# Performance work log

Measured on AMD Instinct MI355X. Metric: run time of the kernel, lower is better.

Reference implementation:

```python
import jax, jax.numpy as jnp
import numpy as np

L = 4  # num GIN layers
HID = 128
B_GRAPHS = 4096

def _bn(x, g, b, m, v):
    return (x - m) / jnp.sqrt(v + 1e-5) * g + b

def _ln(x, g, b):
    mu = jnp.mean(x, axis=-1, keepdims=True)
    var = jnp.var(x, axis=-1, keepdims=True)
    return (x - mu) / jnp.sqrt(var + 1e-5) * g + b

def _gin_encoder(x, ei, bat, aW, ab, eps, W1, b1, g1, be1, m1, v1, W2, b2, g2, be2, m2, v2):
    # x: [N,9], ei: [2,E], bat: [N]
    h = x @ aW + ab                                   # [N,HID]
    src, dst = ei[0], ei[1]
    for l in range(L):
        agg = jnp.zeros_like(h).at[dst].add(h[src])   # scatter-add neighbor sum
        z = (1.0 + eps[l]) * h + agg
        z = jax.nn.relu(_bn(z @ W1[l] + b1[l], g1[l], be1[l], m1[l], v1[l]))
        z = z @ W2[l] + b2[l]
        h = jax.nn.relu(_bn(z, g2[l], be2[l], m2[l], v2[l]))
    sums = jax.ops.segment_sum(h, bat, num_segments=B_GRAPHS)
    cnt = jax.ops.segment_sum(jnp.ones((h.shape[0],), h.dtype), bat, num_segments=B_GRAPHS)
    return sums / jnp.maximum(cnt, 1.0)[:, None]      # global_mean_pool -> [B,HID]

def reference(dx, de, db, sx, se, sb, t,
              enc_atom_W, enc_atom_b, enc_eps, enc_W1, enc_b1,
              enc_bn1_g, enc_bn1_b, enc_bn1_m, enc_bn1_v,
              enc_W2, enc_b2, enc_bn_g, enc_bn_b, enc_bn_m, enc_bn_v,
              temp_W1, temp_b1, temp_W2, temp_b2,
              int_W, int_b, int_ln_g, int_ln_b,
              fus_W1, fus_b1, fus_ln1_g, fus_ln1_b,
              fus_W2, fus_b2, fus_ln2_g, fus_ln2_b, fus_W3, fus_b3):
    # three encoders: [aq(drug), bs(drug), solvent], stacked on leading axis
    xs = jnp.stack([dx, dx, sx])      # [3,N,9]
    eis = jnp.stack([de, de, se])     # [3,2,E]
    bats = jnp.stack([db, db, sb])    # [3,N]
    embs = jax.vmap(_gin_encoder)(xs, eis, bats,
                                  enc_atom_W, enc_atom_b, enc_eps, enc_W1, enc_b1,
                                  enc_bn1_g, enc_bn1_b, enc_bn1_m, enc_bn1_v,
                                  enc_W2, enc_b2, enc_bn_g, enc_bn_b, enc_bn_m, enc_bn_v)
    aq, bs_, so = embs[0], embs[1], embs[2]           # each [B,HID]
    inter = jax.nn.relu(_ln(jnp.concatenate([bs_, so], axis=1) @ int_W + int_b, int_ln_g, int_ln_b))
    temp = jax.nn.relu(t @ temp_W1 + temp_b1) @ temp_W2 + temp_b2
    fusion = jnp.concatenate([aq, inter, temp], axis=1)  # [B, 2*HID+32]
    h = jax.nn.relu(_ln(fusion @ fus_W1 + fus_b1, fus_ln1_g, fus_ln1_b))
    h = jax.nn.relu(_ln(h @ fus_W2 + fus_b2, fus_ln2_g, fus_ln2_b))
    return h @ fus_W3 + fus_b3                        # [B,1]

def setup_inputs() -> dict:
    key = jax.random.key(0)
    ks = jax.random.split(key, 16)
    N, E, B = 50000, 600000, B_GRAPHS
    s = 0.1  # weight scale
    inp = {
        'dx': jax.random.normal(ks[0], (N, 9), jnp.float32),
        'de': jax.random.randint(ks[1], (2, E), 0, N),
        'db': jnp.sort(jax.random.randint(ks[2], (N,), 0, B)),
        'sx': jax.random.normal(ks[3], (N, 9), jnp.float32),
        'se': jax.random.randint(ks[4], (2, E), 0, N),
        'sb': jnp.sort(jax.random.randint(ks[5], (N,), 0, B)),
        't': jax.random.normal(ks[6], (B, 1), jnp.float32),
        'enc_atom_W': jax.random.normal(ks[7], (3, 9, HID), jnp.float32) * s,
        'enc_atom_b': jnp.zeros((3, HID), jnp.float32),
        'enc_eps': jnp.zeros((3, L), jnp.float32),
        'enc_W1': jax.random.normal(ks[8], (3, L, HID, 2 * HID), jnp.float32) * s,
        'enc_b1': jnp.zeros((3, L, 2 * HID), jnp.float32),
        'enc_bn1_g': jnp.ones((3, L, 2 * HID), jnp.float32),
        'enc_bn1_b': jnp.zeros((3, L, 2 * HID), jnp.float32),
        'enc_bn1_m': jnp.zeros((3, L, 2 * HID), jnp.float32),
        'enc_bn1_v': jnp.ones((3, L, 2 * HID), jnp.float32),
        'enc_W2': jax.random.normal(ks[9], (3, L, 2 * HID, HID), jnp.float32) * s,
        'enc_b2': jnp.zeros((3, L, HID), jnp.float32),
        'enc_bn_g': jnp.ones((3, L, HID), jnp.float32),
        'enc_bn_b': jnp.zeros((3, L, HID), jnp.float32),
        'enc_bn_m': jnp.zeros((3, L, HID), jnp.float32),
        'enc_bn_v': jnp.ones((3, L, HID), jnp.float32),
        'temp_W1': jax.random.normal(ks[10], (1, 32), jnp.float32) * s,
        'temp_b1': jnp.zeros((32,), jnp.float32),
        'temp_W2': jax.random.normal(ks[11], (32, 32), jnp.float32) * s,
        'temp_b2': jnp.zeros((32,), jnp.float32),
        'int_W': jax.random.normal(ks[12], (2 * HID, HID), jnp.float32) * s,
        'int_b': jnp.zeros((HID,), jnp.float32),
        'int_ln_g': jnp.ones((HID,), jnp.float32),
        'int_ln_b': jnp.zeros((HID,), jnp.float32),
        'fus_W1': jax.random.normal(ks[13], (2 * HID + 32, HID), jnp.float32) * s,
        'fus_b1': jnp.zeros((HID,), jnp.float32),
        'fus_ln1_g': jnp.ones((HID,), jnp.float32),
        'fus_ln1_b': jnp.zeros((HID,), jnp.float32),
        'fus_W2': jax.random.normal(ks[14], (HID, HID // 2), jnp.float32) * s,
        'fus_b2': jnp.zeros((HID // 2,), jnp.float32),
        'fus_ln2_g': jnp.ones((HID // 2,), jnp.float32),
        'fus_ln2_b': jnp.zeros((HID // 2,), jnp.float32),
        'fus_W3': jax.random.normal(ks[15], (HID // 2, 1), jnp.float32) * s,
        'fus_b3': jnp.zeros((1,), jnp.float32),
    }
    return inp
```

## Files before the change

### kernel.cpp

```cpp
#include <hip/hip_runtime.h>

#define HID 128
#define NLAYER 4

typedef unsigned short u16;
typedef __attribute__((ext_vector_type(8))) unsigned short u16x8;
typedef __attribute__((ext_vector_type(8))) short short8;
typedef __attribute__((ext_vector_type(4))) float floatx4;

__device__ __forceinline__ float bf2f(u16 u) {
    union { unsigned int i; float f; } v; v.i = ((unsigned int)u) << 16; return v.f;
}
__device__ __forceinline__ u16 f2bf(float f) {
    union { float f; unsigned int i; } v; v.f = f;
    unsigned int r = v.i + 0x7FFFu + ((v.i >> 16) & 1u);
    return (u16)(r >> 16);
}

__device__ __forceinline__ int lowbound(const int* __restrict__ a, int n, int v) {
    int lo = 0, hi = n;
    while (lo < hi) {
        int mid = (lo + hi) >> 1;
        if (a[mid] < v) lo = mid + 1; else hi = mid;
    }
    return lo;
}

__global__ void prep_weights(const float* __restrict__ W1, const float* __restrict__ W2,
                             u16* __restrict__ W1t, u16* __restrict__ W2t) {
    const int T = 3 * NLAYER * 128 * 256;
    int o = blockIdx.x * blockDim.x + threadIdx.x;
    if (o < T) {
        int k = o & 127, n = (o >> 7) & 255, el = o >> 15;
        W1t[o] = f2bf(W1[((size_t)el * 128 + k) * 256 + n]);
    } else if (o < 2 * T) {
        int o2 = o - T;
        int k = o2 & 255, n = (o2 >> 8) & 127, el = o2 >> 15;
        W2t[o2] = f2bf(W2[((size_t)el * 256 + k) * 128 + n]);
    }
}

__global__ void hist2(const int* __restrict__ de, const int* __restrict__ se,
                      int* __restrict__ cntd, int* __restrict__ cnts, int Ed, int Es) {
    const int g = blockIdx.y;
    const int* ei = g ? se : de;
    int* cnt = g ? cnts : cntd;
    const int E = g ? Es : Ed;
    int e = blockIdx.x * 256 + threadIdx.x;
    if (e < E) atomicAdd(&cnt[ei[E + e]], 1);
}

__global__ __launch_bounds__(256) void scan1v(const int* __restrict__ cntd,
                                              const int* __restrict__ cnts,
                                              int* __restrict__ bsumd,
                                              int* __restrict__ bsums, int N) {
    const int g = blockIdx.y;
    const int* cnt = g ? cnts : cntd;
    int* bsum = g ? bsums : bsumd;
    __shared__ int s[256];
    int i = blockIdx.x * 256 + threadIdx.x;
    s[threadIdx.x] = (i < N) ? cnt[i] : 0;
    __syncthreads();
    for (int o = 128; o > 0; o >>= 1) {
        if (threadIdx.x < o) s[threadIdx.x] += s[threadIdx.x + o];
        __syncthreads();
    }
    if (threadIdx.x == 0) bsum[blockIdx.x] = s[0];
}

__global__ __launch_bounds__(256) void scan2v(int* __restrict__ bsumd,
                                              int* __restrict__ bsums, int nb) {
    int* bsum = blockIdx.x ? bsums : bsumd;
    __shared__ int s[256];
    __shared__ int carry;
    if (threadIdx.x == 0) carry = 0;
    __syncthreads();
    for (int base = 0; base < nb; base += 256) {
        int i = base + threadIdx.x;
        int v = (i < nb) ? bsum[i] : 0;
        s[threadIdx.x] = v;
        __syncthreads();
        for (int o = 1; o < 256; o <<= 1) {
            int tv = (threadIdx.x >= o) ? s[threadIdx.x - o] : 0;
            __syncthreads();
            s[threadIdx.x] += tv;
            __syncthreads();
        }
        int excl = carry + s[threadIdx.x] - v;
        if (i < nb) bsum[i] = excl;
        __syncthreads();
        if (threadIdx.x == 0) carry += s[255];
        __syncthreads();
    }
}

__global__ __launch_bounds__(256) void scan3v(const int* __restrict__ cntd,
                                              const int* __restrict__ cnts,
                                              const int* __restrict__ bsumd,
                                              const int* __restrict__ bsums,
                                              int* __restrict__ rpd, int* __restrict__ rps,
                                              int* __restrict__ curd, int* __restrict__ curs,
                                              int N, int Ed, int Es) {
    const int g = blockIdx.y;
    const int* cnt = g ? cnts : cntd;
    const int* bsum = g ? bsums : bsumd;
    int* rowptr = g ? rps : rpd;
    int* cur = g ? curs : curd;
    const int E = g ? Es : Ed;
    __shared__ int s[256];
    int i = blockIdx.x * 256 + threadIdx.x;
    int v = (i < N) ? cnt[i] : 0;
    s[threadIdx.x] = v;
    __syncthreads();
    for (int o = 1; o < 256; o <<= 1) {
        int tv = (threadIdx.x >= o) ? s[threadIdx.x - o] : 0;
        __syncthreads();
        s[threadIdx.x] += tv;
        __syncthreads();
    }
    if (i < N) {
        const int st = bsum[blockIdx.x] + s[threadIdx.x] - v;
        rowptr[i] = st;
        cur[i] = st;
    }
    if (i == 0 && blockIdx.x == 0) rowptr[N] = E;
}

__global__ __launch_bounds__(256) void fill2b(const int* __restrict__ de,
                                              const int* __restrict__ se,
                                              int* __restrict__ curd, int* __restrict__ curs,
                                              int* __restrict__ sid, int* __restrict__ sis,
                                              int Ed, int Es, int N) {
    const int g = blockIdx.y;
    const int* ei = g ? se : de;
    int* cur = g ? curs : curd;
    int* srcidx = g ? sis : sid;
    const int E = g ? Es : Ed;
    const int nchunk = gridDim.x >> 3;
    const int bin = blockIdx.x & 7;
    const int chunk = blockIdx.x >> 3;
    const int BS = (N + 7) >> 3;
    const int dlo = bin * BS;
    const int dhi = min(N, dlo + BS);
    const int ce = (E + nchunk - 1) / nchunk;
    const int elo = chunk * ce;
    const int ehi = min(E, elo + ce);
    for (int e = elo + (int)threadIdx.x; e < ehi; e += 256) {
        const int dst = ei[E + e];
        if (dst >= dlo && dst < dhi) {
            const int pos = atomicAdd(&cur[dst], 1);
            srcidx[pos] = ei[e];
        }
    }
}

__global__ void atom_kernel(const float* __restrict__ dx, const float* __restrict__ sx,
                            const float* __restrict__ aW, const float* __restrict__ ab,
                            u16* __restrict__ h, int N) {
    const int slot = blockIdx.z;
    long idx = (long)blockIdx.x * blockDim.x + threadIdx.x;
    if (idx >= (long)N * HID) return;
    const int n = (int)(idx / HID), c = (int)(idx % HID);
    const float* x = (slot < 2) ? dx : sx;
    const float* W = aW + (size_t)slot * 9 * HID;
    float acc = ab[slot * HID + c];
#pragma unroll
    for (int k = 0; k < 9; k++) acc = fmaf(x[n * 9 + k], W[k * HID + c], acc);
    h[(size_t)slot * N * HID + idx] = f2bf(acc);
}

__global__ __launch_bounds__(256) void gather_agg(
    const int* __restrict__ rpd, const int* __restrict__ sid,
    const int* __restrict__ rps, const int* __restrict__ sis,
    const u16* __restrict__ h, u16* __restrict__ z,
    const float* __restrict__ eps, int N, int l) {
    const int slot = blockIdx.z;
    const int node = blockIdx.x * 16 + (threadIdx.x >> 4);
    if (node >= N) return;
    const int lane = threadIdx.x & 63;
    const int sl = lane & 15;
    const int subbase = lane & 48;
    const int* rowptr = (slot < 2) ? rpd : rps;
    const int* srcidx = (slot < 2) ? sid : sis;
    const int lo = rowptr[node], hi = rowptr[node + 1];
    const u16* hp = h + (size_t)slot * N * HID;
    const int coff = sl * 8;

    u16x8 hv = *(const u16x8*)(hp + (size_t)node * HID + coff);
    const float scale = 1.f + eps[slot * NLAYER + l];
    float s[8];
#pragma unroll
    for (int i = 0; i < 8; i++) s[i] = bf2f(hv[i]) * scale;

    for (int base = lo; base < hi; base += 16) {
        const int cnt = min(16, hi - base);
        int idx = (sl < cnt) ? srcidx[base + sl] : 0;
        int j = 0;
        for (; j + 4 <= cnt; j += 4) {
            const int s0 = __shfl(idx, subbase + j);
            const int s1 = __shfl(idx, subbase + j + 1);
            const int s2 = __shfl(idx, subbase + j + 2);
            const int s3 = __shfl(idx, subbase + j + 3);
            u16x8 v0 = *(const u16x8*)(hp + (size_t)s0 * HID + coff);
            u16x8 v1 = *(const u16x8*)(hp + (size_t)s1 * HID + coff);
            u16x8 v2 = *(const u16x8*)(hp + (size_t)s2 * HID + coff);
            u16x8 v3 = *(const u16x8*)(hp + (size_t)s3 * HID + coff);
#pragma unroll
            for (int i = 0; i < 8; i++)
                s[i] += (bf2f(v0[i]) + bf2f(v1[i])) + (bf2f(v2[i]) + bf2f(v3[i]));
        }
        for (; j < cnt; j++) {
            const int sj = __shfl(idx, subbase + j);
            u16x8 v = *(const u16x8*)(hp + (size_t)sj * HID + coff);
#pragma unroll
            for (int i = 0; i < 8; i++) s[i] += bf2f(v[i]);
        }
    }
    u16x8 o;
#pragma unroll
    for (int i = 0; i < 8; i++) o[i] = f2bf(s[i]);
    *(u16x8*)(z + (size_t)slot * N * HID + (size_t)node * HID + coff) = o;
}

__global__ __launch_bounds__(256, 2) void fused_layer(
    const u16* __restrict__ A, const u16* __restrict__ W1t, const u16* __restrict__ W2t,
    const float* __restrict__ b1, const float* __restrict__ g1, const float* __restrict__ be1,
    const float* __restrict__ m1, const float* __restrict__ v1,
    const float* __restrict__ b2, const float* __restrict__ g2, const float* __restrict__ be2,
    const float* __restrict__ m2, const float* __restrict__ v2,
    u16* __restrict__ out, int M, int l) {

    const int slot = blockIdx.z;
    const int m0 = blockIdx.x * 128;
    const u16* Ap  = A + (size_t)slot * M * 128;
    const int el = slot * NLAYER + l;
    const u16* Wp1 = W1t + (size_t)el * (256 * 128);
    const u16* Wp2 = W2t + (size_t)el * (128 * 256);
    const size_t poff1 = (size_t)el * 256;
    const size_t poff2 = (size_t)el * 128;

    __shared__ u16 sm[128 * 136];

    const int tid = threadIdx.x;
    const int lane = tid & 63;
    const int w = tid >> 6;
    const int sl = lane & 15;
    const int k8 = lane >> 4;

    {
        const int rp = tid >> 4;
        const int kc = (tid & 15) * 8;
#pragma unroll
        for (int p = 0; p < 8; p++) {
            const int row = p * 16 + rp;
            int gr = m0 + row; if (gr >= M) gr = M - 1;
            *(uint4*)&sm[row * 136 + kc] = *(const uint4*)(Ap + (size_t)gr * 128 + kc);
        }
    }
    __syncthreads();

    floatx4 acc1[8][4];
#pragma unroll
    for (int mt = 0; mt < 8; mt++)
#pragma unroll
        for (int c = 0; c < 4; c++) acc1[mt][c] = (floatx4)0.f;

#pragma unroll
    for (int ks = 0; ks < 4; ks++) {
        short8 a[8], b[4];
#pragma unroll
        for (int mt = 0; mt < 8; mt++)
            a[mt] = *(const short8*)&sm[(mt * 16 + sl) * 136 + ks * 32 + k8 * 8];
#pragma unroll
        for (int c = 0; c < 4; c++) {
            const int n = (c * 4 + w) * 16 + sl;
            b[c] = *(const short8*)(Wp1 + (size_t)n * 128 + ks * 32 + k8 * 8);
        }
#pragma unroll
        for (int mt = 0; mt < 8; mt++)
#pragma unroll
            for (int c = 0; c < 4; c++)
                acc1[mt][c] = __builtin_amdgcn_mfma_f32_16x16x32_bf16(a[mt], b[c], acc1[mt][c], 0, 0, 0);
    }
    __syncthreads();

    const int wr = w & 1, wc = w >> 1;
    floatx4 acc2[4][4];
#pragma unroll
    for (int mt = 0; mt < 4; mt++)
#pragma unroll
        for (int nt = 0; nt < 4; nt++) acc2[mt][nt] = (floatx4)0.f;

#pragma unroll
    for (int part = 0; part < 2; part++) {
#pragma unroll
        for (int c = part * 2; c < part * 2 + 2; c++) {
            const int gcol = (c * 4 + w) * 16 + sl;
            const int lcol = gcol - part * 128;
            const float sc = g1[poff1 + gcol] * rsqrtf(v1[poff1 + gcol] + 1e-5f);
            const float sh = (b1[poff1 + gcol] - m1[poff1 + gcol]) * sc + be1[poff1 + gcol];
#pragma unroll
            for (int mt = 0; mt < 8; mt++) {
#pragma unroll
                for (int r = 0; r < 4; r++) {
                    const int m = mt * 16 + k8 * 4 + r;
                    sm[m * 136 + lcol] = f2bf(fmaxf(fmaf(acc1[mt][c][r], sc, sh), 0.f));
                }
            }
        }
        __syncthreads();
#pragma unroll
        for (int ks = 0; ks < 4; ks++) {
            short8 a[4], b[4];
#pragma unroll
            for (int mt = 0; mt < 4; mt++)
                a[mt] = *(const short8*)&sm[(wr * 64 + mt * 16 + sl) * 136 + ks * 32 + k8 * 8];
#pragma unroll
            for (int nt = 0; nt < 4; nt++) {
                const int n = wc * 64 + nt * 16 + sl;
                b[nt] = *(const short8*)(Wp2 + (size_t)n * 256 + part * 128 + ks * 32 + k8 * 8);
            }
#pragma unroll
            for (int mt = 0; mt < 4; mt++)
#pragma unroll
                for (int nt = 0; nt < 4; nt++)
                    acc2[mt][nt] = __builtin_amdgcn_mfma_f32_16x16x32_bf16(a[mt], b[nt], acc2[mt][nt], 0, 0, 0);
        }
        if (part == 0) __syncthreads();
    }

    u16* outp = out + (size_t)slot * M * 128;
#pragma unroll
    for (int nt = 0; nt < 4; nt++) {
        const int col = wc * 64 + nt * 16 + sl;
        const float sc = g2[poff2 + col] * rsqrtf(v2[poff2 + col] + 1e-5f);
        const float sh = (b2[poff2 + col] - m2[poff2 + col]) * sc + be2[poff2 + col];
#pragma unroll
        for (int mt = 0; mt < 4; mt++) {
#pragma unroll
            for (int r = 0; r < 4; r++) {
                const int gr = m0 + wr * 64 + mt * 16 + k8 * 4 + r;
                if (gr < M)
                    outp[(size_t)gr * 128 + col] = f2bf(fmaxf(fmaf(acc2[mt][nt][r], sc, sh), 0.f));
            }
        }
    }
}

__global__ __launch_bounds__(128) void pool_kernel(const int* __restrict__ db,
                                                   const int* __restrict__ sb,
                                                   const u16* __restrict__ h,
                                                   float* __restrict__ emb,
                                                   int N, int B) {
    const int slot = blockIdx.z;
    const int* bat = (slot < 2) ? db : sb;
    const int g = blockIdx.x;
    const int lo = lowbound(bat, N, g);
    const int hi = lowbound(bat, N, g + 1);
    const int c = threadIdx.x;
    float s = 0.f;
    const u16* hp = h + (size_t)slot * N * HID;
    for (int n = lo; n < hi; n++) s += bf2f(hp[(size_t)n * HID + c]);
    const float cnt = (float)(hi - lo);
    emb[((size_t)slot * B + g) * HID + c] = s / fmaxf(cnt, 1.f);
}

__device__ __forceinline__ float block_sum128(float x, float* red, int tid) {
    red[tid] = x;
    __syncthreads();
    if (tid < 64) {
        float v = red[tid] + red[tid + 64];
#pragma unroll
        for (int o = 32; o > 0; o >>= 1) v += __shfl_down(v, o);
        if (tid == 0) red[0] = v;
    }
    __syncthreads();
    float r = red[0];
    __syncthreads();
    return r;
}

__global__ __launch_bounds__(128) void fusion_kernel(
    const float* __restrict__ emb, const float* __restrict__ t,
    const float* __restrict__ tW1, const float* __restrict__ tb1,
    const float* __restrict__ tW2, const float* __restrict__ tb2,
    const float* __restrict__ iW, const float* __restrict__ ib,
    const float* __restrict__ ilg, const float* __restrict__ ilb,
    const float* __restrict__ fW1, const float* __restrict__ fb1,
    const float* __restrict__ l1g, const float* __restrict__ l1b,
    const float* __restrict__ fW2, const float* __restrict__ fb2,
    const float* __restrict__ l2g, const float* __restrict__ l2b,
    const float* __restrict__ fW3, const float* __restrict__ fb3,
    float* __restrict__ out, int B) {
    const int r = blockIdx.x;
    const int tid = threadIdx.x;
    __shared__ float cs[256];
    __shared__ float cat[288];
    __shared__ float buf[128];
    __shared__ float red[128];
    __shared__ float tmp32[32];

    cs[tid]        = emb[((size_t)1 * B + r) * HID + tid];
    cs[128 + tid]  = emb[((size_t)2 * B + r) * HID + tid];
    cat[tid]       = emb[((size_t)0 * B + r) * HID + tid];
    __syncthreads();

    float acc = ib[tid];
    for (int k = 0; k < 256; k++) acc = fmaf(cs[k], iW[k * HID + tid], acc);
    float mu  = block_sum128(acc, red, tid) * (1.f / 128.f);
    float d   = acc - mu;
    float var = block_sum128(d * d, red, tid) * (1.f / 128.f);
    float inter = fmaxf(d * rsqrtf(var + 1e-5f) * ilg[tid] + ilb[tid], 0.f);
    cat[128 + tid] = inter;

    if (tid < 32) tmp32[tid] = fmaxf(fmaf(t[r], tW1[tid], tb1[tid]), 0.f);
    __syncthreads();
    if (tid < 32) {
        float a2 = tb2[tid];
        for (int j = 0; j < 32; j++) a2 = fmaf(tmp32[j], tW2[j * 32 + tid], a2);
        cat[256 + tid] = a2;
    }
    __syncthreads();

    float a1 = fb1[tid];
    for (int k = 0; k < 288; k++) a1 = fmaf(cat[k], fW1[k * HID + tid], a1);
    mu  = block_sum128(a1, red, tid) * (1.f / 128.f);
    d   = a1 - mu;
    var = block_sum128(d * d, red, tid) * (1.f / 128.f);
    buf[tid] = fmaxf(d * rsqrtf(var + 1e-5f) * l1g[tid] + l1b[tid], 0.f);
    __syncthreads();

    float a2v = 0.f;
    if (tid < 64) {
        a2v = fb2[tid];
        for (int k = 0; k < 128; k++) a2v = fmaf(buf[k], fW2[k * 64 + tid], a2v);
    }
    mu = block_sum128((tid < 64) ? a2v : 0.f, red, tid) * (1.f / 64.f);
    float d2 = (tid < 64) ? (a2v - mu) : 0.f;
    var = block_sum128(d2 * d2, red, tid) * (1.f / 64.f);
    float contrib = 0.f;
    if (tid < 64) {
        float h2 = fmaxf(d2 * rsqrtf(var + 1e-5f) * l2g[tid] + l2b[tid], 0.f);
        contrib = h2 * fW3[tid];
    }
    float s = block_sum128(contrib, red, tid);
    if (tid == 0) out[r] = s + fb3[0];
}

extern "C" void kernel_launch(void* const* d_in, const int* in_sizes, int n_in,
                              void* d_out, int out_size, void* d_ws, size_t ws_size,
                              hipStream_t stream) {
    const float* dx  = (const float*)d_in[0];
    const int*   de  = (const int*)d_in[1];
    const int*   db  = (const int*)d_in[2];
    const float* sx  = (const float*)d_in[3];
    const int*   se  = (const int*)d_in[4];
    const int*   sb  = (const int*)d_in[5];
    const float* t   = (const float*)d_in[6];
    const float* aW  = (const float*)d_in[7];
    const float* ab  = (const float*)d_in[8];
    const float* eps = (const float*)d_in[9];
    const float* W1  = (const float*)d_in[10];
    const float* b1  = (const float*)d_in[11];
    const float* g1  = (const float*)d_in[12];
    const float* be1 = (const float*)d_in[13];
    const float* m1  = (const float*)d_in[14];
    const float* v1  = (const float*)d_in[15];
    const float* W2  = (const float*)d_in[16];
    const float* b2  = (const float*)d_in[17];
    const float* g2  = (const float*)d_in[18];
    const float* be2 = (const float*)d_in[19];
    const float* m2  = (const float*)d_in[20];
    const float* v2  = (const float*)d_in[21];
    const float* tW1 = (const float*)d_in[22];
    const float* tb1 = (const float*)d_in[23];
    const float* tW2 = (const float*)d_in[24];
    const float* tb2 = (const float*)d_in[25];
    const float* iW  = (const float*)d_in[26];
    const float* ib  = (const float*)d_in[27];
    const float* ilg = (const float*)d_in[28];
    const float* ilb = (const float*)d_in[29];
    const float* fW1 = (const float*)d_in[30];
    const float* fb1 = (const float*)d_in[31];
    const float* l1g = (const float*)d_in[32];
    const float* l1b = (const float*)d_in[33];
    const float* fW2 = (const float*)d_in[34];
    const float* fb2 = (const float*)d_in[35];
    const float* l2g = (const float*)d_in[36];
    const float* l2b = (const float*)d_in[37];
    const float* fW3 = (const float*)d_in[38];
    const float* fb3 = (const float*)d_in[39];
    float* out = (float*)d_out;

    const int N  = in_sizes[0] / 9;
    const int Ed = in_sizes[1] / 2;
    const int Es = in_sizes[4] / 2;
    const int B  = in_sizes[6];
    const int nb = (N + 255) / 256;

    char* w8 = (char*)d_ws;
    int* rpd   = (int*)w8;
    int* rps   = rpd + (N + 1);
    int* cntd  = rps + (N + 1);
    int* cnts  = cntd + N;
    int* curd  = cnts + N;
    int* curs  = curd + N;
    int* sid   = curs + N;
    int* sis   = sid + Ed;
    int* bsumd = sis + Es;
    int* bsums = bsumd + nb;
    size_t int_bytes = ((char*)(bsums + nb)) - w8;
    size_t foff = (int_bytes + 255) & ~(size_t)255;

    const int WT = 3 * NLAYER * 128 * 256;
    u16* W1t = (u16*)(w8 + foff);
    u16* W2t = W1t + WT;
    const size_t hS = (size_t)N * HID;
    u16* hbuf = W2t + WT;
    u16* zbuf = hbuf + 3 * hS;
    float* emb = (float*)(((uintptr_t)(zbuf + 3 * hS) + 255) & ~(uintptr_t)255);

    prep_weights<<<(2 * WT + 255) / 256, 256, 0, stream>>>(W1, W2, W1t, W2t);
    hipMemsetAsync(cntd, 0, (size_t)2 * N * sizeof(int), stream);
    {
        const int Emax = (Ed > Es) ? Ed : Es;
        dim3 gh((Emax + 255) / 256, 2);
        hist2<<<gh, 256, 0, stream>>>(de, se, cntd, cnts, Ed, Es);
        dim3 gs1(nb, 2);
        scan1v<<<gs1, 256, 0, stream>>>(cntd, cnts, bsumd, bsums, N);
        scan2v<<<2, 256, 0, stream>>>(bsumd, bsums, nb);
        scan3v<<<gs1, 256, 0, stream>>>(cntd, cnts, bsumd, bsums, rpd, rps, curd, curs, N, Ed, Es);
        dim3 gfb(128 * 8, 2);
        fill2b<<<gfb, 256, 0, stream>>>(de, se, curd, curs, sid, sis, Ed, Es, N);
    }

    {
        dim3 ga((N * HID + 255) / 256, 1, 3);
        atom_kernel<<<ga, 256, 0, stream>>>(dx, sx, aW, ab, hbuf, N);
        for (int l = 0; l < NLAYER; l++) {
            dim3 gg((N + 15) / 16, 1, 3);
            gather_agg<<<gg, 256, 0, stream>>>(rpd, sid, rps, sis, hbuf, zbuf, eps, N, l);
            dim3 gf((N + 127) / 128, 1, 3);
            fused_layer<<<gf, 256, 0, stream>>>(zbuf, W1t, W2t,
                                                b1, g1, be1, m1, v1,
                                                b2, g2, be2, m2, v2,
                                                hbuf, N, l);
        }
        dim3 gp(B, 1, 3);
        pool_kernel<<<gp, 128, 0, stream>>>(db, sb, hbuf, emb, N, B);
    }
    fusion_kernel<<<B, 128, 0, stream>>>(emb, t, tW1, tb1, tW2, tb2,
                                         iW, ib, ilg, ilb, fW1, fb1, l1g, l1b,
                                         fW2, fb2, l2g, l2b, fW3, fb3, out, B);
}
```

Baseline: 826.5 us.

## Interleave the two drug encoders' features so one gather serves both slots

Node features for the two drug encoders, which share the same graph, are stored interleaved as 256-wide rows. The aggregation kernel now walks the drug CSR once and sums both encoders' neighbour rows in a single pass, while solvent nodes are handled in a second z-slice. This removes the duplicate index reads and traversal for the shared drug graph and makes each neighbour fetch a contiguous 512-byte row. The dense layer and pooling kernels take a row stride to read and write this layout. The cost is more registers per thread and a 2-way unroll instead of 4-way in the drug path.

```diff
diff --git a/kernel.cpp b/kernel.cpp
--- a/kernel.cpp
+++ b/kernel.cpp
@@ -156,7 +156,7 @@
 
 __global__ void atom_kernel(const float* __restrict__ dx, const float* __restrict__ sx,
                             const float* __restrict__ aW, const float* __restrict__ ab,
-                            u16* __restrict__ h, int N) {
+                            u16* __restrict__ h01, u16* __restrict__ h2, int N) {
     const int slot = blockIdx.z;
     long idx = (long)blockIdx.x * blockDim.x + threadIdx.x;
     if (idx >= (long)N * HID) return;
@@ -166,73 +166,121 @@
     float acc = ab[slot * HID + c];
 #pragma unroll
     for (int k = 0; k < 9; k++) acc = fmaf(x[n * 9 + k], W[k * HID + c], acc);
-    h[(size_t)slot * N * HID + idx] = f2bf(acc);
-}
-
-__global__ __launch_bounds__(256) void gather_agg(
+    if (slot < 2) h01[(size_t)n * 256 + slot * 128 + c] = f2bf(acc);
+    else          h2[(size_t)n * 128 + c] = f2bf(acc);
+}
+
+__global__ __launch_bounds__(256) void gather_agg2(
     const int* __restrict__ rpd, const int* __restrict__ sid,
     const int* __restrict__ rps, const int* __restrict__ sis,
-    const u16* __restrict__ h, u16* __restrict__ z,
+    const u16* __restrict__ h01, const u16* __restrict__ h2,
+    u16* __restrict__ z01, u16* __restrict__ z2,
     const float* __restrict__ eps, int N, int l) {
-    const int slot = blockIdx.z;
+    const int pz = blockIdx.z;
     const int node = blockIdx.x * 16 + (threadIdx.x >> 4);
     if (node >= N) return;
     const int lane = threadIdx.x & 63;
     const int sl = lane & 15;
     const int subbase = lane & 48;
-    const int* rowptr = (slot < 2) ? rpd : rps;
-    const int* srcidx = (slot < 2) ? sid : sis;
-    const int lo = rowptr[node], hi = rowptr[node + 1];
-    const u16* hp = h + (size_t)slot * N * HID;
     const int coff = sl * 8;
 
-    u16x8 hv = *(const u16x8*)(hp + (size_t)node * HID + coff);
-    const float scale = 1.f + eps[slot * NLAYER + l];
-    float s[8];
-#pragma unroll
-    for (int i = 0; i < 8; i++) s[i] = bf2f(hv[i]) * scale;
-
-    for (int base = lo; base < hi; base += 16) {
-        const int cnt = min(16, hi - base);
-        int idx = (sl < cnt) ? srcidx[base + sl] : 0;
-        int j = 0;
-        for (; j + 4 <= cnt; j += 4) {
-            const int s0 = __shfl(idx, subbase + j);
-            const int s1 = __shfl(idx, subbase + j + 1);
-            const int s2 = __shfl(idx, subbase + j + 2);
-            const int s3 = __shfl(idx, subbase + j + 3);
-            u16x8 v0 = *(const u16x8*)(hp + (size_t)s0 * HID + coff);
-            u16x8 v1 = *(const u16x8*)(hp + (size_t)s1 * HID + coff);
-            u16x8 v2 = *(const u16x8*)(hp + (size_t)s2 * HID + coff);
-            u16x8 v3 = *(const u16x8*)(hp + (size_t)s3 * HID + coff);
-#pragma unroll
-            for (int i = 0; i < 8; i++)
-                s[i] += (bf2f(v0[i]) + bf2f(v1[i])) + (bf2f(v2[i]) + bf2f(v3[i]));
-        }
-        for (; j < cnt; j++) {
-            const int sj = __shfl(idx, subbase + j);
-            u16x8 v = *(const u16x8*)(hp + (size_t)sj * HID + coff);
-#pragma unroll
-            for (int i = 0; i < 8; i++) s[i] += bf2f(v[i]);
-        }
-    }
-    u16x8 o;
-#pragma unroll
-    for (int i = 0; i < 8; i++) o[i] = f2bf(s[i]);
-    *(u16x8*)(z + (size_t)slot * N * HID + (size_t)node * HID + coff) = o;
+    if (pz == 0) {
+        const int lo = rpd[node], hi = rpd[node + 1];
+        const float sc0 = 1.f + eps[0 * NLAYER + l];
+        const float sc1 = 1.f + eps[1 * NLAYER + l];
+        float s0[8], s1[8];
+        {
+            u16x8 a0 = *(const u16x8*)(h01 + (size_t)node * 256 + coff);
+            u16x8 a1 = *(const u16x8*)(h01 + (size_t)node * 256 + 128 + coff);
+#pragma unroll
+            for (int i = 0; i < 8; i++) { s0[i] = bf2f(a0[i]) * sc0; s1[i] = bf2f(a1[i]) * sc1; }
+        }
+        for (int base = lo; base < hi; base += 16) {
+            const int cnt = min(16, hi - base);
+            int idx = (sl < cnt) ? sid[base + sl] : 0;
+            int j = 0;
+            for (; j + 2 <= cnt; j += 2) {
+                const int e0 = __shfl(idx, subbase + j);
+                const int e1 = __shfl(idx, subbase + j + 1);
+                u16x8 v00 = *(const u16x8*)(h01 + (size_t)e0 * 256 + coff);
+                u16x8 v01 = *(const u16x8*)(h01 + (size_t)e0 * 256 + 128 + coff);
+                u16x8 v10 = *(const u16x8*)(h01 + (size_t)e1 * 256 + coff);
+                u16x8 v11 = *(const u16x8*)(h01 + (size_t)e1 * 256 + 128 + coff);
+#pragma unroll
+                for (int i = 0; i < 8; i++) {
+                    s0[i] += bf2f(v00[i]) + bf2f(v10[i]);
+                    s1[i] += bf2f(v01[i]) + bf2f(v11[i]);
+                }
+            }
+            for (; j < cnt; j++) {
+                const int e0 = __shfl(idx, subbase + j);
+                u16x8 v0 = *(const u16x8*)(h01 + (size_t)e0 * 256 + coff);
+                u16x8 v1 = *(const u16x8*)(h01 + (size_t)e0 * 256 + 128 + coff);
+#pragma unroll
+                for (int i = 0; i < 8; i++) { s0[i] += bf2f(v0[i]); s1[i] += bf2f(v1[i]); }
+            }
+        }
+        u16x8 o0, o1;
+#pragma unroll
+        for (int i = 0; i < 8; i++) { o0[i] = f2bf(s0[i]); o1[i] = f2bf(s1[i]); }
+        *(u16x8*)(z01 + (size_t)node * 256 + coff) = o0;
+        *(u16x8*)(z01 + (size_t)node * 256 + 128 + coff) = o1;
+    } else {
+        const int lo = rps[node], hi = rps[node + 1];
+        const float scale = 1.f + eps[2 * NLAYER + l];
+        float s[8];
+        {
+            u16x8 hv = *(const u16x8*)(h2 + (size_t)node * 128 + coff);
+#pragma unroll
+            for (int i = 0; i < 8; i++) s[i] = bf2f(hv[i]) * scale;
+        }
+        for (int base = lo; base < hi; base += 16) {
+            const int cnt = min(16, hi - base);
+            int idx = (sl < cnt) ? sis[base + sl] : 0;
+            int j = 0;
+            for (; j + 4 <= cnt; j += 4) {
+                const int e0 = __shfl(idx, subbase + j);
+                const int e1 = __shfl(idx, subbase + j + 1);
+                const int e2 = __shfl(idx, subbase + j + 2);
+                const int e3 = __shfl(idx, subbase + j + 3);
+                u16x8 v0 = *(const u16x8*)(h2 + (size_t)e0 * 128 + coff);
+                u16x8 v1 = *(const u16x8*)(h2 + (size_t)e1 * 128 + coff);
+                u16x8 v2 = *(const u16x8*)(h2 + (size_t)e2 * 128 + coff);
+                u16x8 v3 = *(const u16x8*)(h2 + (size_t)e3 * 128 + coff);
+#pragma unroll
+                for (int i = 0; i < 8; i++)
+                    s[i] += (bf2f(v0[i]) + bf2f(v1[i])) + (bf2f(v2[i]) + bf2f(v3[i]));
+            }
+            for (; j < cnt; j++) {
+                const int e0 = __shfl(idx, subbase + j);
+                u16x8 v = *(const u16x8*)(h2 + (size_t)e0 * 128 + coff);
+#pragma unroll
+                for (int i = 0; i < 8; i++) s[i] += bf2f(v[i]);
+            }
+        }
+        u16x8 o;
+#pragma unroll
+        for (int i = 0; i < 8; i++) o[i] = f2bf(s[i]);
+        *(u16x8*)(z2 + (size_t)node * 128 + coff) = o;
+    }
 }
 
 __global__ __launch_bounds__(256, 2) void fused_layer(
-    const u16* __restrict__ A, const u16* __restrict__ W1t, const u16* __restrict__ W2t,
+    const u16* __restrict__ A01, const u16* __restrict__ A2,
+    const u16* __restrict__ W1t, const u16* __restrict__ W2t,
     const float* __restrict__ b1, const float* __restrict__ g1, const float* __restrict__ be1,
     const float* __restrict__ m1, const float* __restrict__ v1,
     const float* __restrict__ b2, const float* __restrict__ g2, const float* __restrict__ be2,
     const float* __restrict__ m2, const float* __restrict__ v2,
-    u16* __restrict__ out, int M, int l) {
+    u16* __restrict__ out01, u16* __restrict__ out2, int M, int l) {
 
     const int slot = blockIdx.z;
     const int m0 = blockIdx.x * 128;
-    const u16* Ap  = A + (size_t)slot * M * 128;
+    const u16* Ap;
+    u16* outp;
+    int rs;
+    if (slot < 2) { Ap = A01 + slot * 128; outp = out01 + slot * 128; rs = 256; }
+    else          { Ap = A2;               outp = out2;               rs = 128; }
     const int el = slot * NLAYER + l;
     const u16* Wp1 = W1t + (size_t)el * (256 * 128);
     const u16* Wp2 = W2t + (size_t)el * (128 * 256);
@@ -254,7 +302,7 @@
         for (int p = 0; p < 8; p++) {
             const int row = p * 16 + rp;
             int gr = m0 + row; if (gr >= M) gr = M - 1;
-            *(uint4*)&sm[row * 136 + kc] = *(const uint4*)(Ap + (size_t)gr * 128 + kc);
+            *(uint4*)&sm[row * 136 + kc] = *(const uint4*)(Ap + (size_t)gr * rs + kc);
         }
     }
     __syncthreads();
@@ -329,7 +377,6 @@
         if (part == 0) __syncthreads();
     }
 
-    u16* outp = out + (size_t)slot * M * 128;
 #pragma unroll
     for (int nt = 0; nt < 4; nt++) {
         const int col = wc * 64 + nt * 16 + sl;
@@ -341,7 +388,7 @@
             for (int r = 0; r < 4; r++) {
                 const int gr = m0 + wr * 64 + mt * 16 + k8 * 4 + r;
                 if (gr < M)
-                    outp[(size_t)gr * 128 + col] = f2bf(fmaxf(fmaf(acc2[mt][nt][r], sc, sh), 0.f));
+                    outp[(size_t)gr * rs + col] = f2bf(fmaxf(fmaf(acc2[mt][nt][r], sc, sh), 0.f));
             }
         }
     }
@@ -349,7 +396,8 @@
 
 __global__ __launch_bounds__(128) void pool_kernel(const int* __restrict__ db,
                                                    const int* __restrict__ sb,
-                                                   const u16* __restrict__ h,
+                                                   const u16* __restrict__ h01,
+                                                   const u16* __restrict__ h2,
                                                    float* __restrict__ emb,
                                                    int N, int B) {
     const int slot = blockIdx.z;
@@ -359,8 +407,12 @@
     const int hi = lowbound(bat, N, g + 1);
     const int c = threadIdx.x;
     float s = 0.f;
-    const u16* hp = h + (size_t)slot * N * HID;
-    for (int n = lo; n < hi; n++) s += bf2f(hp[(size_t)n * HID + c]);
+    if (slot < 2) {
+        const u16* hp = h01 + slot * 128;
+        for (int n = lo; n < hi; n++) s += bf2f(hp[(size_t)n * 256 + c]);
+    } else {
+        for (int n = lo; n < hi; n++) s += bf2f(h2[(size_t)n * 128 + c]);
+    }
     const float cnt = (float)(hi - lo);
     emb[((size_t)slot * B + g) * HID + c] = s / fmaxf(cnt, 1.f);
 }
@@ -536,18 +588,22 @@
 
     {
         dim3 ga((N * HID + 255) / 256, 1, 3);
-        atom_kernel<<<ga, 256, 0, stream>>>(dx, sx, aW, ab, hbuf, N);
+        atom_kernel<<<ga, 256, 0, stream>>>(dx, sx, aW, ab, hbuf, hbuf + 2 * hS, N);
+        u16* cur = hbuf;
+        u16* nxt = zbuf;
         for (int l = 0; l < NLAYER; l++) {
-            dim3 gg((N + 15) / 16, 1, 3);
-            gather_agg<<<gg, 256, 0, stream>>>(rpd, sid, rps, sis, hbuf, zbuf, eps, N, l);
+            dim3 gg((N + 15) / 16, 1, 2);
+            gather_agg2<<<gg, 256, 0, stream>>>(rpd, sid, rps, sis,
+                                                cur, cur + 2 * hS,
+                                                nxt, nxt + 2 * hS, eps, N, l);
             dim3 gf((N + 127) / 128, 1, 3);
-            fused_layer<<<gf, 256, 0, stream>>>(zbuf, W1t, W2t,
+            fused_layer<<<gf, 256, 0, stream>>>(nxt, nxt + 2 * hS, W1t, W2t,
                                                 b1, g1, be1, m1, v1,
                                                 b2, g2, be2, m2, v2,
-                                                hbuf, N, l);
+                                                cur, cur + 2 * hS, N, l);
         }
         dim3 gp(B, 1, 3);
-        pool_kernel<<<gp, 128, 0, stream>>>(db, sb, hbuf, emb, N, B);
+        pool_kernel<<<gp, 128, 0, stream>>>(db, sb, hbuf, hbuf + 2 * hS, emb, N, B);
     }
     fusion_kernel<<<B, 128, 0, stream>>>(emb, t, tW1, tb1, tW2, tb2,
                                          iW, ib, ilg, ilb, fW1, fb1, l1g, l1b,
```

Measured after the change: 874.4 us. 1.06x slower.

## Halve fused_layer row tile and interleave GEMM1 halves to cut registers

Applied to the files above, without the earlier changes.

The fused MLP layer kernel now processes 64 rows per block instead of 128 and computes the first GEMM in two 128-column halves, each immediately feeding the second GEMM, with separate shared buffers for the input tile and the hidden activations. This shrinks accumulator register usage (acc1 8x4 down to 4x2, acc2 4x4 down to 2x4), so the launch bound rises to 4 blocks per SM and the grid doubles. The aim is higher occupancy and more blocks for latency hiding. The cost is that each weight tile is reloaded from global or cache memory twice as often per row.

```diff
diff --git a/kernel.cpp b/kernel.cpp
--- a/kernel.cpp
+++ b/kernel.cpp
@@ -222,7 +222,7 @@
     *(u16x8*)(z + (size_t)slot * N * HID + (size_t)node * HID + coff) = o;
 }
 
-__global__ __launch_bounds__(256, 2) void fused_layer(
+__global__ __launch_bounds__(256, 4) void fused_layer(
     const u16* __restrict__ A, const u16* __restrict__ W1t, const u16* __restrict__ W2t,
     const float* __restrict__ b1, const float* __restrict__ g1, const float* __restrict__ be1,
     const float* __restrict__ m1, const float* __restrict__ v1,
@@ -231,7 +231,7 @@
     u16* __restrict__ out, int M, int l) {
 
     const int slot = blockIdx.z;
-    const int m0 = blockIdx.x * 128;
+    const int m0 = blockIdx.x * 64;
     const u16* Ap  = A + (size_t)slot * M * 128;
     const int el = slot * NLAYER + l;
     const u16* Wp1 = W1t + (size_t)el * (256 * 128);
@@ -239,7 +239,8 @@
     const size_t poff1 = (size_t)el * 256;
     const size_t poff2 = (size_t)el * 128;
 
-    __shared__ u16 sm[128 * 136];
+    __shared__ u16 smz[64 * 136];
+    __shared__ u16 smz2[64 * 136];
 
     const int tid = threadIdx.x;
     const int lane = tid & 63;
@@ -251,80 +252,80 @@
         const int rp = tid >> 4;
         const int kc = (tid & 15) * 8;
 #pragma unroll
-        for (int p = 0; p < 8; p++) {
+        for (int p = 0; p < 4; p++) {
             const int row = p * 16 + rp;
             int gr = m0 + row; if (gr >= M) gr = M - 1;
-            *(uint4*)&sm[row * 136 + kc] = *(const uint4*)(Ap + (size_t)gr * 128 + kc);
-        }
-    }
-    __syncthreads();
-
-    floatx4 acc1[8][4];
-#pragma unroll
-    for (int mt = 0; mt < 8; mt++)
-#pragma unroll
-        for (int c = 0; c < 4; c++) acc1[mt][c] = (floatx4)0.f;
-
-#pragma unroll
-    for (int ks = 0; ks < 4; ks++) {
-        short8 a[8], b[4];
-#pragma unroll
-        for (int mt = 0; mt < 8; mt++)
-            a[mt] = *(const short8*)&sm[(mt * 16 + sl) * 136 + ks * 32 + k8 * 8];
-#pragma unroll
-        for (int c = 0; c < 4; c++) {
-            const int n = (c * 4 + w) * 16 + sl;
-            b[c] = *(const short8*)(Wp1 + (size_t)n * 128 + ks * 32 + k8 * 8);
-        }
-#pragma unroll
-        for (int mt = 0; mt < 8; mt++)
-#pragma unroll
-            for (int c = 0; c < 4; c++)
-                acc1[mt][c] = __builtin_amdgcn_mfma_f32_16x16x32_bf16(a[mt], b[c], acc1[mt][c], 0, 0, 0);
+            *(uint4*)&smz[row * 136 + kc] = *(const uint4*)(Ap + (size_t)gr * 128 + kc);
+        }
     }
     __syncthreads();
 
     const int wr = w & 1, wc = w >> 1;
-    floatx4 acc2[4][4];
-#pragma unroll
-    for (int mt = 0; mt < 4; mt++)
+    floatx4 acc2[2][4];
+#pragma unroll
+    for (int mt = 0; mt < 2; mt++)
 #pragma unroll
         for (int nt = 0; nt < 4; nt++) acc2[mt][nt] = (floatx4)0.f;
 
 #pragma unroll
     for (int part = 0; part < 2; part++) {
-#pragma unroll
-        for (int c = part * 2; c < part * 2 + 2; c++) {
-            const int gcol = (c * 4 + w) * 16 + sl;
+        floatx4 acc1[4][2];
+#pragma unroll
+        for (int mt = 0; mt < 4; mt++)
+#pragma unroll
+            for (int cc = 0; cc < 2; cc++) acc1[mt][cc] = (floatx4)0.f;
+
+#pragma unroll
+        for (int ks = 0; ks < 4; ks++) {
+            short8 a[4], b[2];
+#pragma unroll
+            for (int mt = 0; mt < 4; mt++)
+                a[mt] = *(const short8*)&smz[(mt * 16 + sl) * 136 + ks * 32 + k8 * 8];
+#pragma unroll
+            for (int cc = 0; cc < 2; cc++) {
+                const int n = ((part * 2 + cc) * 4 + w) * 16 + sl;
+                b[cc] = *(const short8*)(Wp1 + (size_t)n * 128 + ks * 32 + k8 * 8);
+            }
+#pragma unroll
+            for (int mt = 0; mt < 4; mt++)
+#pragma unroll
+                for (int cc = 0; cc < 2; cc++)
+                    acc1[mt][cc] = __builtin_amdgcn_mfma_f32_16x16x32_bf16(a[mt], b[cc], acc1[mt][cc], 0, 0, 0);
+        }
+
+#pragma unroll
+        for (int cc = 0; cc < 2; cc++) {
+            const int gcol = ((part * 2 + cc) * 4 + w) * 16 + sl;
             const int lcol = gcol - part * 128;
             const float sc = g1[poff1 + gcol] * rsqrtf(v1[poff1 + gcol] + 1e-5f);
             const float sh = (b1[poff1 + gcol] - m1[poff1 + gcol]) * sc + be1[poff1 + gcol];
 #pragma unroll
-            for (int mt = 0; mt < 8; mt++) {
+            for (int mt = 0; mt < 4; mt++) {
 #pragma unroll
                 for (int r = 0; r < 4; r++) {
                     const int m = mt * 16 + k8 * 4 + r;
-                    sm[m * 136 + lcol] = f2bf(fmaxf(fmaf(acc1[mt][c][r], sc, sh), 0.f));
+                    smz2[m * 136 + lcol] = f2bf(fmaxf(fmaf(acc1[mt][cc][r], sc, sh), 0.f));
                 }
             }
         }
         __syncthreads();
+
 #pragma unroll
         for (int ks = 0; ks < 4; ks++) {
-            short8 a[4], b[4];
-#pragma unroll
-            for (int mt = 0; mt < 4; mt++)
-                a[mt] = *(const short8*)&sm[(wr * 64 + mt * 16 + sl) * 136 + ks * 32 + k8 * 8];
+            short8 a2[2], b2[4];
+#pragma unroll
+            for (int mt = 0; mt < 2; mt++)
+                a2[mt] = *(const short8*)&smz2[(wr * 32 + mt * 16 + sl) * 136 + ks * 32 + k8 * 8];
 #pragma unroll
             for (int nt = 0; nt < 4; nt++) {
                 const int n = wc * 64 + nt * 16 + sl;
-                b[nt] = *(const short8*)(Wp2 + (size_t)n * 256 + part * 128 + ks * 32 + k8 * 8);
+                b2[nt] = *(const short8*)(Wp2 + (size_t)n * 256 + part * 128 + ks * 32 + k8 * 8);
             }
 #pragma unroll
-            for (int mt = 0; mt < 4; mt++)
+            for (int mt = 0; mt < 2; mt++)
 #pragma unroll
                 for (int nt = 0; nt < 4; nt++)
-                    acc2[mt][nt] = __builtin_amdgcn_mfma_f32_16x16x32_bf16(a[mt], b[nt], acc2[mt][nt], 0, 0, 0);
+                    acc2[mt][nt] = __builtin_amdgcn_mfma_f32_16x16x32_bf16(a2[mt], b2[nt], acc2[mt][nt], 0, 0, 0);
         }
         if (part == 0) __syncthreads();
     }
@@ -336,10 +337,10 @@
         const float sc = g2[poff2 + col] * rsqrtf(v2[poff2 + col] + 1e-5f);
         const float sh = (b2[poff2 + col] - m2[poff2 + col]) * sc + be2[poff2 + col];
 #pragma unroll
-        for (int mt = 0; mt < 4; mt++) {
+        for (int mt = 0; mt < 2; mt++) {
 #pragma unroll
             for (int r = 0; r < 4; r++) {
-                const int gr = m0 + wr * 64 + mt * 16 + k8 * 4 + r;
+                const int gr = m0 + wr * 32 + mt * 16 + k8 * 4 + r;
                 if (gr < M)
                     outp[(size_t)gr * 128 + col] = f2bf(fmaxf(fmaf(acc2[mt][nt][r], sc, sh), 0.f));
             }
@@ -540,7 +541,7 @@
         for (int l = 0; l < NLAYER; l++) {
             dim3 gg((N + 15) / 16, 1, 3);
             gather_agg<<<gg, 256, 0, stream>>>(rpd, sid, rps, sis, hbuf, zbuf, eps, N, l);
-            dim3 gf((N + 127) / 128, 1, 3);
+            dim3 gf((N + 63) / 64, 1, 3);
             fused_layer<<<gf, 256, 0, stream>>>(zbuf, W1t, W2t,
                                                 b1, g1, be1, m1, v1,
                                                 b2, g2, be2, m2, v2,
```

Result: slower. 933.8 us (+13.0%).

## Stage GEMM weights through LDS and bin histogram atomics by destination range

Applied to the files above, without the earlier changes.

The fused layer kernel now loads W1 and W2 tiles cooperatively into a padded shared-memory buffer before the MFMA loops, instead of having each wave read B fragments straight from global memory. This is meant to cut redundant global and L2 weight traffic. The cost is more LDS per block, which may lower occupancy, plus extra barriers. Separately, the degree histogram is rewritten to use 8 destination bins over edge chunks, like fill2b, so atomics stay within a node range. That bin split makes each edge get read 8 times.

```diff
diff --git a/kernel.cpp b/kernel.cpp
--- a/kernel.cpp
+++ b/kernel.cpp
@@ -40,14 +40,27 @@
     }
 }
 
-__global__ void hist2(const int* __restrict__ de, const int* __restrict__ se,
-                      int* __restrict__ cntd, int* __restrict__ cnts, int Ed, int Es) {
+__global__ __launch_bounds__(256) void hist2b(const int* __restrict__ de,
+                                              const int* __restrict__ se,
+                                              int* __restrict__ cntd, int* __restrict__ cnts,
+                                              int Ed, int Es, int N) {
     const int g = blockIdx.y;
     const int* ei = g ? se : de;
     int* cnt = g ? cnts : cntd;
     const int E = g ? Es : Ed;
-    int e = blockIdx.x * 256 + threadIdx.x;
-    if (e < E) atomicAdd(&cnt[ei[E + e]], 1);
+    const int nchunk = gridDim.x >> 3;
+    const int bin = blockIdx.x & 7;
+    const int chunk = blockIdx.x >> 3;
+    const int BS = (N + 7) >> 3;
+    const int dlo = bin * BS;
+    const int dhi = min(N, dlo + BS);
+    const int ce = (E + nchunk - 1) / nchunk;
+    const int elo = chunk * ce;
+    const int ehi = min(E, elo + ce);
+    for (int e = elo + (int)threadIdx.x; e < ehi; e += 256) {
+        const int dst = ei[E + e];
+        if (dst >= dlo && dst < dhi) atomicAdd(&cnt[dst], 1);
+    }
 }
 
 __global__ __launch_bounds__(256) void scan1v(const int* __restrict__ cntd,
@@ -239,7 +252,8 @@
     const size_t poff1 = (size_t)el * 256;
     const size_t poff2 = (size_t)el * 128;
 
-    __shared__ u16 sm[128 * 136];
+    __shared__ u16 smz[128 * 136];
+    __shared__ u16 smw[256 * 72];
 
     const int tid = threadIdx.x;
     const int lane = tid & 63;
@@ -254,8 +268,14 @@
         for (int p = 0; p < 8; p++) {
             const int row = p * 16 + rp;
             int gr = m0 + row; if (gr >= M) gr = M - 1;
-            *(uint4*)&sm[row * 136 + kc] = *(const uint4*)(Ap + (size_t)gr * 128 + kc);
-        }
+            *(uint4*)&smz[row * 136 + kc] = *(const uint4*)(Ap + (size_t)gr * 128 + kc);
+        }
+    }
+#pragma unroll
+    for (int it = 0; it < 8; it++) {
+        const int ch = it * 256 + tid;
+        const int row = ch >> 3, kc = ch & 7;
+        *(uint4*)&smw[row * 72 + kc * 8] = *(const uint4*)(Wp1 + (size_t)row * 128 + kc * 8);
     }
     __syncthreads();
 
@@ -266,21 +286,35 @@
         for (int c = 0; c < 4; c++) acc1[mt][c] = (floatx4)0.f;
 
 #pragma unroll
-    for (int ks = 0; ks < 4; ks++) {
-        short8 a[8], b[4];
-#pragma unroll
-        for (int mt = 0; mt < 8; mt++)
-            a[mt] = *(const short8*)&sm[(mt * 16 + sl) * 136 + ks * 32 + k8 * 8];
-#pragma unroll
-        for (int c = 0; c < 4; c++) {
-            const int n = (c * 4 + w) * 16 + sl;
-            b[c] = *(const short8*)(Wp1 + (size_t)n * 128 + ks * 32 + k8 * 8);
-        }
-#pragma unroll
-        for (int mt = 0; mt < 8; mt++)
-#pragma unroll
-            for (int c = 0; c < 4; c++)
-                acc1[mt][c] = __builtin_amdgcn_mfma_f32_16x16x32_bf16(a[mt], b[c], acc1[mt][c], 0, 0, 0);
+    for (int hh = 0; hh < 2; hh++) {
+        if (hh == 1) {
+            __syncthreads();
+#pragma unroll
+            for (int it = 0; it < 8; it++) {
+                const int ch = it * 256 + tid;
+                const int row = ch >> 3, kc = ch & 7;
+                *(uint4*)&smw[row * 72 + kc * 8] = *(const uint4*)(Wp1 + (size_t)row * 128 + 64 + kc * 8);
+            }
+            __syncthreads();
+        }
+#pragma unroll
+        for (int ksl = 0; ksl < 2; ksl++) {
+            const int ks = hh * 2 + ksl;
+            short8 a[8], b[4];
+#pragma unroll
+            for (int mt = 0; mt < 8; mt++)
+                a[mt] = *(const short8*)&smz[(mt * 16 + sl) * 136 + ks * 32 + k8 * 8];
+#pragma unroll
+            for (int c = 0; c < 4; c++) {
+                const int n = (c * 4 + w) * 16 + sl;
+                b[c] = *(const short8*)&smw[n * 72 + ksl * 32 + k8 * 8];
+            }
+#pragma unroll
+            for (int mt = 0; mt < 8; mt++)
+#pragma unroll
+                for (int c = 0; c < 4; c++)
+                    acc1[mt][c] = __builtin_amdgcn_mfma_f32_16x16x32_bf16(a[mt], b[c], acc1[mt][c], 0, 0, 0);
+        }
     }
     __syncthreads();
 
@@ -304,21 +338,27 @@
 #pragma unroll
                 for (int r = 0; r < 4; r++) {
                     const int m = mt * 16 + k8 * 4 + r;
-                    sm[m * 136 + lcol] = f2bf(fmaxf(fmaf(acc1[mt][c][r], sc, sh), 0.f));
+                    smz[m * 136 + lcol] = f2bf(fmaxf(fmaf(acc1[mt][c][r], sc, sh), 0.f));
                 }
             }
         }
+#pragma unroll
+        for (int it = 0; it < 8; it++) {
+            const int ch = it * 256 + tid;
+            const int row = ch >> 4, kc = ch & 15;
+            *(uint4*)&smw[row * 136 + kc * 8] = *(const uint4*)(Wp2 + (size_t)row * 256 + part * 128 + kc * 8);
+        }
         __syncthreads();
 #pragma unroll
         for (int ks = 0; ks < 4; ks++) {
             short8 a[4], b[4];
 #pragma unroll
             for (int mt = 0; mt < 4; mt++)
-                a[mt] = *(const short8*)&sm[(wr * 64 + mt * 16 + sl) * 136 + ks * 32 + k8 * 8];
+                a[mt] = *(const short8*)&smz[(wr * 64 + mt * 16 + sl) * 136 + ks * 32 + k8 * 8];
 #pragma unroll
             for (int nt = 0; nt < 4; nt++) {
                 const int n = wc * 64 + nt * 16 + sl;
-                b[nt] = *(const short8*)(Wp2 + (size_t)n * 256 + part * 128 + ks * 32 + k8 * 8);
+                b[nt] = *(const short8*)&smw[n * 136 + ks * 32 + k8 * 8];
             }
 #pragma unroll
             for (int mt = 0; mt < 4; mt++)
@@ -523,15 +563,13 @@
     prep_weights<<<(2 * WT + 255) / 256, 256, 0, stream>>>(W1, W2, W1t, W2t);
     hipMemsetAsync(cntd, 0, (size_t)2 * N * sizeof(int), stream);
     {
-        const int Emax = (Ed > Es) ? Ed : Es;
-        dim3 gh((Emax + 255) / 256, 2);
-        hist2<<<gh, 256, 0, stream>>>(de, se, cntd, cnts, Ed, Es);
+        dim3 gb(128 * 8, 2);
+        hist2b<<<gb, 256, 0, stream>>>(de, se, cntd, cnts, Ed, Es, N);
         dim3 gs1(nb, 2);
         scan1v<<<gs1, 256, 0, stream>>>(cntd, cnts, bsumd, bsums, N);
         scan2v<<<2, 256, 0, stream>>>(bsumd, bsums, nb);
         scan3v<<<gs1, 256, 0, stream>>>(cntd, cnts, bsumd, bsums, rpd, rps, curd, curs, N, Ed, Es);
-        dim3 gfb(128 * 8, 2);
-        fill2b<<<gfb, 256, 0, stream>>>(de, se, curd, curs, sid, sis, Ed, Es, N);
+        fill2b<<<gb, 256, 0, stream>>>(de, se, curd, curs, sid, sis, Ed, Es, N);
     }
 
     {
```

Result: faster. 781.8 us (-5.4%).
